# Kernel tuning notes

Measured on AMD Instinct MI355X. Metric: run time of the kernel, lower is better.

Reference implementation:

```python
import jax, jax.numpy as jnp
import numpy as np

V, E, H, K, B, T = 32000, 128, 256, 9, 64, 512


def setup_inputs() -> dict:
    key = jax.random.key(0)
    ks = jax.random.split(key, 12)
    text = jax.random.randint(ks[0], (B, T), 1, V, dtype=jnp.int32)
    lens = jax.random.randint(ks[1], (B,), T // 4, T + 1)
    text = jnp.where(jnp.arange(T)[None, :] < lens[:, None], text, 0)  # 0 = PAD
    labels = jax.random.randint(ks[2], (B, T), 0, K, dtype=jnp.int32)
    g = lambda k, shape, s: jax.random.normal(k, shape, jnp.float32) * s
    emb = g(ks[3], (V, E), 0.02)
    Wf, Uf, bf = g(ks[4], (E, 4 * H), 0.05), g(ks[5], (H, 4 * H), 0.05), jnp.zeros((4 * H,), jnp.float32)
    Wb, Ub, bb = g(ks[6], (E, 4 * H), 0.05), g(ks[7], (H, 4 * H), 0.05), jnp.zeros((4 * H,), jnp.float32)
    Wd, bd = g(ks[8], (2 * H, K), 0.05), jnp.zeros((K,), jnp.float32)
    trans = jax.random.uniform(ks[9], (K, K), jnp.float32)
    return dict(text=text, labels=labels, emb=emb, Wf=Wf, Uf=Uf, bf=bf,
                Wb=Wb, Ub=Ub, bb=bb, Wd=Wd, bd=bd, trans=trans)


def _lstm(x, W, U, b):
    # x: [B, T, E]; Keras LSTM gate order i, f, g(cell), o
    Hn = U.shape[0]
    Bn = x.shape[0]

    def step(carry, xt):
        h, c = carry
        z = xt @ W + h @ U + b
        i, f, g, o = jnp.split(z, 4, axis=-1)
        c = jax.nn.sigmoid(f) * c + jax.nn.sigmoid(i) * jnp.tanh(g)
        h = jax.nn.sigmoid(o) * jnp.tanh(c)
        return (h, c), h

    init = (jnp.zeros((Bn, Hn), x.dtype), jnp.zeros((Bn, Hn), x.dtype))
    _, hs = jax.lax.scan(step, init, jnp.swapaxes(x, 0, 1))  # [T, B, H]
    return jnp.swapaxes(hs, 0, 1)


def _crf_log_likelihood(logits, labels, lens, trans):
    # logits: [B, T, K], labels: [B, T] int, lens: [B] int, trans: [K, K]
    Bn, Tn, Kn = logits.shape
    tmask = jnp.arange(Tn)[None, :] < lens[:, None]           # [B, T] valid token
    tmask2 = jnp.arange(1, Tn)[None, :] < lens[:, None]       # [B, T-1] valid transition
    # gold score: unary + binary
    unary = jnp.take_along_axis(logits, labels[..., None], axis=-1)[..., 0]  # [B, T]
    unary_sum = jnp.sum(unary * tmask, axis=-1)
    binary = trans[labels[:, :-1], labels[:, 1:]]             # [B, T-1]
    binary_sum = jnp.sum(binary * tmask2, axis=-1)
    # log partition via forward algorithm (masked scan)
    alpha0 = logits[:, 0]                                     # [B, K]

    def step(alpha, inp):
        logit_t, m_t = inp                                    # [B, K], [B]
        new = jax.nn.logsumexp(alpha[:, :, None] + trans[None], axis=1) + logit_t
        alpha = jnp.where(m_t[:, None], new, alpha)
        return alpha, None

    alpha, _ = jax.lax.scan(step, alpha0,
                            (jnp.swapaxes(logits[:, 1:], 0, 1), tmask2.T))
    log_norm = jax.nn.logsumexp(alpha, axis=-1)               # [B]
    return unary_sum + binary_sum - log_norm


def reference(text, labels, emb, Wf, Uf, bf, Wb, Ub, bb, Wd, bd, trans):
    text_lens = jnp.sum((text != 0).astype(jnp.int32), axis=-1)
    x = emb[text]                                             # [B, T, E]; dropout inactive at inference
    hf = _lstm(x, Wf, Uf, bf)
    hb = _lstm(x[:, ::-1], Wb, Ub, bb)[:, ::-1]
    logits = jnp.concatenate([hf, hb], axis=-1) @ Wd + bd     # [B, T, K]
    ll = _crf_log_likelihood(logits, labels, text_lens, trans)
    return logits, text_lens, ll
```

## Files before the change

### kernel.cpp

```cpp
#include <hip/hip_runtime.h>
#include <math.h>

#define T_LEN  512
#define B_SZ   64
#define E_DIM  128
#define H_DIM  256
#define G4     1024
#define K_TAGS 9
#define HP     268

typedef __bf16 bf16x8 __attribute__((ext_vector_type(8)));
typedef float  f32x4  __attribute__((ext_vector_type(4)));

union BF8 { bf16x8 v; unsigned short u[8]; uint4 q; unsigned long long ull[2]; };

__device__ __forceinline__ unsigned short rne_bf16(float x) {
    unsigned int b = __float_as_uint(x);
    b += 0x7FFFu + ((b >> 16) & 1u);
    return (unsigned short)(b >> 16);
}
__device__ __forceinline__ float bf16_to_f(unsigned short u) {
    return __uint_as_float(((unsigned int)u) << 16);
}
__device__ __forceinline__ float rcpf_(float x)  { return __builtin_amdgcn_rcpf(x); }
__device__ __forceinline__ float sigf(float x)   { return rcpf_(1.0f + __expf(-x)); }
__device__ __forceinline__ float tanhf_(float x) { return fmaf(2.0f, rcpf_(1.0f + __expf(-2.0f * x)), -1.0f); }

__global__ __launch_bounds__(256)
void init_kernel(const int* __restrict__ text, const float* __restrict__ bd,
                 float* __restrict__ out, int* __restrict__ ws_head) {
    const int b   = blockIdx.x;
    const int tid = threadIdx.x;
    float* lb = out + (size_t)b * (T_LEN * K_TAGS);
    for (int i = tid; i < T_LEN * K_TAGS; i += 256) lb[i] = bd[i % K_TAGS];
    int cnt = 0;
    for (int t = tid; t < T_LEN; t += 256) cnt += (text[b * T_LEN + t] != 0) ? 1 : 0;
    __shared__ int red[4];
    for (int off = 32; off > 0; off >>= 1) cnt += __shfl_down(cnt, off);
    if ((tid & 63) == 0) red[tid >> 6] = cnt;
    __syncthreads();
    if (tid == 0) {
        int c = red[0] + red[1] + red[2] + red[3];
        out[(size_t)B_SZ * T_LEN * K_TAGS + b] = (float)c;
        ws_head[b] = c;
    }
}

__global__ __launch_bounds__(64)
void permute_kernel(const float* __restrict__ Wf, const float* __restrict__ Uf, const float* __restrict__ bf_,
                    const float* __restrict__ Wb, const float* __restrict__ Ub, const float* __restrict__ bb,
                    unsigned short* __restrict__ Uc, unsigned short* __restrict__ Wc,
                    float* __restrict__ bperm)
{
    const int colp = blockIdx.x;
    const int dir  = blockIdx.y;
    const float* W = dir ? Wb : Wf;
    const float* U = dir ? Ub : Uf;
    const float* bs = dir ? bb : bf_;
    const int g = colp & 3, u = colp >> 2;
    const int oc = g * 256 + u;
    const int t = threadIdx.x;
    for (int k = t; k < 256; k += 64)
        Uc[((size_t)dir * 1024 + colp) * 256 + k] = rne_bf16(U[(size_t)k * G4 + oc]);
    for (int k = t; k < 128; k += 64)
        Wc[((size_t)dir * 1024 + colp) * 128 + k] = rne_bf16(W[(size_t)k * G4 + oc]);
    if (t == 0) bperm[dir * 1024 + colp] = bs[oc];
}

__global__ __launch_bounds__(512)
void xw_kernel(const int* __restrict__ text, const float* __restrict__ emb,
               const unsigned short* __restrict__ Wc, const float* __restrict__ bperm,
               unsigned short* __restrict__ xwq)
{
    const int t   = blockIdx.x;
    const int dir = blockIdx.y;
    const int tid = threadIdx.x;
    const int w = tid >> 6, l = tid & 63, r = l & 15, q = l >> 4;

    __shared__ unsigned short xs[64][136];
    __shared__ unsigned short wl[256][136];

    {
        const int b = tid >> 3, e0 = (tid & 7) * 16;
        const int tok = text[b * T_LEN + t];
        const float* er = emb + (size_t)tok * E_DIM + e0;
        #pragma unroll
        for (int jj = 0; jj < 16; ++jj) xs[b][e0 + jj] = rne_bf16(er[jj]);
    }

    for (int nc = 0; nc < 4; ++nc) {
        __syncthreads();
        for (int i = tid; i < 256 * 16; i += 512) {
            const int cc = i >> 4, k8 = (i & 15) * 8;
            *(uint4*)&wl[cc][k8] =
                *(const uint4*)&Wc[((size_t)dir * 1024 + 256 * nc + cc) * 128 + k8];
        }
        __syncthreads();

        #pragma unroll
        for (int mt = 0; mt < 2; ++mt) {
            const int ccol = 32 * w + 16 * mt + r;
            const float4 bb4 = *(const float4*)&bperm[dir * 1024 + 256 * nc + 32 * w + 16 * mt + 4 * q];
            f32x4 acc[4];
            #pragma unroll
            for (int nt = 0; nt < 4; ++nt) acc[nt] = (f32x4){bb4.x, bb4.y, bb4.z, bb4.w};
            #pragma unroll
            for (int ks = 0; ks < 4; ++ks) {
                BF8 af; af.q = *(const uint4*)&wl[ccol][32 * ks + 8 * q];
                #pragma unroll
                for (int nt = 0; nt < 4; ++nt) {
                    BF8 bfv; bfv.q = *(const uint4*)&xs[16 * nt + r][32 * ks + 8 * q];
                    acc[nt] = __builtin_amdgcn_mfma_f32_16x16x32_bf16(af.v, bfv.v, acc[nt], 0, 0, 0);
                }
            }
            #pragma unroll
            for (int nt = 0; nt < 4; ++nt) {
                const int quad = 64 * nc + 8 * w + 4 * mt + q;
                unsigned long long pv =
                      (unsigned long long)rne_bf16(acc[nt][0])
                    | ((unsigned long long)rne_bf16(acc[nt][1]) << 16)
                    | ((unsigned long long)rne_bf16(acc[nt][2]) << 32)
                    | ((unsigned long long)rne_bf16(acc[nt][3]) << 48);
                const size_t off = ((((size_t)dir * 4 + nt) * T_LEN + t) * 256 + quad) * 16 + r;
                *(unsigned long long*)&xwq[off * 4] = pv;
            }
        }
    }
}

__global__ __launch_bounds__(512, 1)
void rec_kernel(const unsigned short* __restrict__ Uc,
                unsigned short* __restrict__ xwq)
{
    const int bx  = blockIdx.x;
    const int dir = bx >> 2, bq = bx & 3;
    const int tid = threadIdx.x;
    const int w = tid >> 6, l = tid & 63, r = l & 15, q = l >> 4;

    __shared__ uint4 ulds4[2][4][1024];
    __shared__ unsigned short hlds[2][16][HP];

    const unsigned short* ucb = Uc + (size_t)dir * 1024 * 256;

    BF8 uf[8][5];
    #pragma unroll
    for (int nt = 0; nt < 8; ++nt) {
        const int colp = 128 * w + 16 * nt + r;
        #pragma unroll
        for (int ks = 0; ks < 5; ++ks)
            uf[nt][ks].q = *(const uint4*)&ucb[(size_t)colp * 256 + 32 * ks + 8 * q];
    }
    for (int i = tid; i < 8192; i += 512) {
        const int s = i >> 12, qq = (i >> 10) & 3, colp = i & 1023;
        ulds4[s][qq][colp] =
            *(const uint4*)&ucb[(size_t)colp * 256 + 160 + 32 * s + 8 * qq];
    }
    {
        unsigned int* hz = (unsigned int*)&hlds[0][0][0];
        for (int i = tid; i < 16 * HP / 2; i += 512) hz[i] = 0u;
    }
    float creg[8] = {0.f, 0.f, 0.f, 0.f, 0.f, 0.f, 0.f, 0.f};
    uint4 hpack = make_uint4(0, 0, 0, 0);
    unsigned short* xwb = xwq + (size_t)(dir * 4 + bq) * T_LEN * 16384;
    const size_t hoff = (size_t)(((w * 4 + q) * 16 + r) * 8);
    __syncthreads();

    for (int t = 0; t < T_LEN; ++t) {
        const int Rb = t & 1, Wn = Rb ^ 1;

        if (t > 0)
            *(uint4*)&xwb[(size_t)(t - 1) * 16384 + hoff] = hpack;

        #pragma unroll
        for (int gr = 0; gr < 2; ++gr) {
            uint2 xwv[4];
            BF8   u7[4];
            #pragma unroll
            for (int nn = 0; nn < 4; ++nn) {
                const int nt = 4 * gr + nn;
                const int quad = 32 * w + 4 * nt + q;
                xwv[nn] = *(const uint2*)&xwb[(size_t)t * 16384 + (size_t)(quad * 16 + r) * 4];
                const int colp = 128 * w + 16 * nt + r;
                u7[nn].q = *(const uint4*)&ucb[(size_t)colp * 256 + 224 + 8 * q];
            }

            f32x4 acc[4];
            #pragma unroll
            for (int nn = 0; nn < 4; ++nn) acc[nn] = (f32x4){0.f, 0.f, 0.f, 0.f};
            #pragma unroll
            for (int ks = 0; ks < 5; ++ks) {
                BF8 hfv; hfv.q = *(const uint4*)&hlds[Rb][r][32 * ks + 8 * q];
                #pragma unroll
                for (int nn = 0; nn < 4; ++nn)
                    acc[nn] = __builtin_amdgcn_mfma_f32_16x16x32_bf16(
                        uf[4 * gr + nn][ks].v, hfv.v, acc[nn], 0, 0, 0);
            }
            #pragma unroll
            for (int ks = 5; ks < 7; ++ks) {
                BF8 hfv; hfv.q = *(const uint4*)&hlds[Rb][r][32 * ks + 8 * q];
                #pragma unroll
                for (int nn = 0; nn < 4; ++nn) {
                    const int colp = 128 * w + 16 * (4 * gr + nn) + r;
                    BF8 uv; uv.q = ulds4[ks - 5][q][colp];
                    acc[nn] = __builtin_amdgcn_mfma_f32_16x16x32_bf16(uv.v, hfv.v, acc[nn], 0, 0, 0);
                }
            }
            {
                BF8 hfv; hfv.q = *(const uint4*)&hlds[Rb][r][224 + 8 * q];
                #pragma unroll
                for (int nn = 0; nn < 4; ++nn)
                    acc[nn] = __builtin_amdgcn_mfma_f32_16x16x32_bf16(
                        u7[nn].v, hfv.v, acc[nn], 0, 0, 0);
            }

            unsigned int p0 = 0, p1 = 0;
            #pragma unroll
            for (int nn = 0; nn < 4; ++nn) {
                const int nt = 4 * gr + nn;
                const uint2 xv = xwv[nn];
                const float z0 = acc[nn][0] + bf16_to_f((unsigned short)(xv.x & 0xffff));
                const float z1 = acc[nn][1] + bf16_to_f((unsigned short)(xv.x >> 16));
                const float z2 = acc[nn][2] + bf16_to_f((unsigned short)(xv.y & 0xffff));
                const float z3 = acc[nn][3] + bf16_to_f((unsigned short)(xv.y >> 16));
                const float c = sigf(z1) * creg[nt] + sigf(z0) * tanhf_(z2);
                const float h = sigf(z3) * tanhf_(c);
                creg[nt] = c;
                const unsigned short hh = rne_bf16(h);
                hlds[Wn][r][32 * w + 4 * nt + q] = hh;
                if (nn < 2) p0 |= ((unsigned int)hh) << (16 * (nn & 1));
                else        p1 |= ((unsigned int)hh) << (16 * (nn & 1));
            }
            if (gr == 0) { hpack.x = p0; hpack.y = p1; }
            else         { hpack.z = p0; hpack.w = p1; }
        }
        __syncthreads();
    }
    *(uint4*)&xwb[(size_t)(T_LEN - 1) * 16384 + hoff] = hpack;
}

__global__ __launch_bounds__(256)
void logits_kernel(const unsigned short* __restrict__ xwq,
                   const float* __restrict__ Wd, const float* __restrict__ bd,
                   float* __restrict__ out)
{
    __shared__ float wdl[2 * H_DIM * K_TAGS];
    __shared__ float bdl[16];
    const int tid = threadIdx.x;
    for (int i = tid; i < 2 * H_DIM * K_TAGS; i += 256) wdl[i] = Wd[i];
    if (tid < K_TAGS) bdl[tid] = bd[tid];
    __syncthreads();

    const int flat = blockIdx.x * 256 + tid;
    const int b = flat >> 9, t = flat & (T_LEN - 1);
    const int bq = b >> 4, bl = b & 15;
    const unsigned short* hf = xwq + ((size_t)(0 * 4 + bq) * T_LEN + t) * 16384;
    const unsigned short* hb = xwq + ((size_t)(1 * 4 + bq) * T_LEN + (T_LEN - 1 - t)) * 16384;

    float a[K_TAGS];
    #pragma unroll
    for (int k = 0; k < K_TAGS; ++k) a[k] = bdl[k];
    #pragma unroll
    for (int w = 0; w < 8; ++w) {
        #pragma unroll
        for (int q = 0; q < 4; ++q) {
            BF8 hv; hv.q = *(const uint4*)&hf[((w * 4 + q) * 16 + bl) * 8];
            #pragma unroll
            for (int nt = 0; nt < 8; ++nt) {
                const float h = bf16_to_f(hv.u[nt]);
                const float* wr = &wdl[(32 * w + 4 * nt + q) * K_TAGS];
                #pragma unroll
                for (int k = 0; k < K_TAGS; ++k) a[k] = fmaf(h, wr[k], a[k]);
            }
        }
    }
    #pragma unroll
    for (int w = 0; w < 8; ++w) {
        #pragma unroll
        for (int q = 0; q < 4; ++q) {
            BF8 hv; hv.q = *(const uint4*)&hb[((w * 4 + q) * 16 + bl) * 8];
            #pragma unroll
            for (int nt = 0; nt < 8; ++nt) {
                const float h = bf16_to_f(hv.u[nt]);
                const float* wr = &wdl[(H_DIM + 32 * w + 4 * nt + q) * K_TAGS];
                #pragma unroll
                for (int k = 0; k < K_TAGS; ++k) a[k] = fmaf(h, wr[k], a[k]);
            }
        }
    }
    float* ob = out + ((size_t)b * T_LEN + t) * K_TAGS;
    #pragma unroll
    for (int k = 0; k < K_TAGS; ++k) ob[k] = a[k];
}

__global__ __launch_bounds__(1024)
void lstm_fb(const int* __restrict__ text, const float* __restrict__ emb,
             const float* __restrict__ Wf, const float* __restrict__ Uf, const float* __restrict__ bf_,
             const float* __restrict__ Wb, const float* __restrict__ Ub, const float* __restrict__ bb,
             const float* __restrict__ Wd, float* __restrict__ out)
{
    const int bi   = blockIdx.x;
    const int d    = bi >> 5;
    const int pair = bi & 31;
    const int tid  = threadIdx.x;
    const int kc   = tid >> 8;
    const int idx  = tid & 255;

    const float* Wp = d ? Wb : Wf;
    const float* Up = d ? Ub : Uf;
    const float* bp = d ? bb : bf_;

    __shared__ __align__(16) float2 vbuf[2][384];
    __shared__ float  cspf[2][H_DIM];
    __shared__ __align__(16) float2 zp[16][256];
    __shared__ float  wdl[H_DIM * K_TAGS];
    __shared__ float  bpl[G4];

    for (int i = tid; i < H_DIM * K_TAGS; i += 1024) wdl[i] = Wd[d * H_DIM * K_TAGS + i];
    for (int i = tid; i < G4; i += 1024) bpl[i] = bp[i];
    if (tid < H_DIM) {
        vbuf[0][E_DIM + tid] = make_float2(0.0f, 0.0f);
        cspf[0][tid] = 0.0f;
        cspf[1][tid] = 0.0f;
    }
    __syncthreads();

    int cur = 0;
    for (int t = 0; t < T_LEN; ++t) {
        const int p = d ? (T_LEN - 1 - t) : t;
        const int nxt = cur ^ 1;

        if (tid < E_DIM) {
            const int tok0 = text[(pair * 2 + 0) * T_LEN + p];
            const int tok1 = text[(pair * 2 + 1) * T_LEN + p];
            vbuf[cur][tid] = make_float2(emb[(size_t)tok0 * E_DIM + tid],
                                         emb[(size_t)tok1 * E_DIM + tid]);
        }
        __syncthreads();

        {
            float2 a0 = make_float2(0.f, 0.f), a1 = a0, a2 = a0, a3 = a0;
            const int k0 = kc * 96;
            const float* wp = Wp + (size_t)k0 * G4 + 4 * idx;
            const float* up = Up + ((long)k0 - E_DIM) * G4 + 4 * idx;
            const float2* __restrict__ vb = vbuf[cur];
            #pragma unroll 8
            for (int i = 0; i < 96; ++i) {
                const int k = k0 + i;
                const float4 wv = *(const float4*)((k < E_DIM) ? wp : up);
                const float2 v = vb[k];
                a0.x = fmaf(wv.x, v.x, a0.x); a0.y = fmaf(wv.x, v.y, a0.y);
                a1.x = fmaf(wv.y, v.x, a1.x); a1.y = fmaf(wv.y, v.y, a1.y);
                a2.x = fmaf(wv.z, v.x, a2.x); a2.y = fmaf(wv.z, v.y, a2.y);
                a3.x = fmaf(wv.w, v.x, a3.x); a3.y = fmaf(wv.w, v.y, a3.y);
                wp += G4; up += G4;
            }
            zp[kc * 4 + 0][idx] = a0;
            zp[kc * 4 + 1][idx] = a1;
            zp[kc * 4 + 2][idx] = a2;
            zp[kc * 4 + 3][idx] = a3;
        }
        __syncthreads();

        if (tid < 512) {
            const int b = tid >> 8, u = tid & 255;
            const int j = u & 3, rr = u >> 2;
            float zs[4];
            #pragma unroll
            for (int g = 0; g < 4; ++g) {
                float s = bpl[g * 256 + u];
                #pragma unroll
                for (int c = 0; c < 4; ++c)
                    s += ((const float*)&zp[c * 4 + j][g * 64 + rr])[b];
                zs[g] = s;
            }
            const float co = cspf[b][u];
            const float cg = tanhf_(zs[2]);
            const float cn = sigf(zs[1]) * co + sigf(zs[0]) * cg;
            const float h  = sigf(zs[3]) * tanhf_(cn);
            cspf[b][u] = cn;
            ((float*)&vbuf[nxt][E_DIM + u])[b] = h;
        }
        __syncthreads();

        {
            const int w = tid >> 6, l = tid & 63;
            const float2* __restrict__ hb = vbuf[nxt] + E_DIM;
            for (int tau = w; tau < 2 * K_TAGS; tau += 16) {
                const int gb = tau / K_TAGS, k = tau - K_TAGS * gb;
                float v = 0.0f;
                #pragma unroll
                for (int m = 0; m < 4; ++m) {
                    const int col = l + 64 * m;
                    const float hv = ((const float*)&hb[col])[gb];
                    v += hv * wdl[col * K_TAGS + k];
                }
                for (int off = 32; off > 0; off >>= 1) v += __shfl_down(v, off);
                if (l == 0)
                    atomicAdd(&out[((size_t)(pair * 2 + gb) * T_LEN + p) * K_TAGS + k], v);
            }
        }
        cur = nxt;
    }
}

__global__ __launch_bounds__(64)
void crf_kernel(const int* __restrict__ labels, const float* __restrict__ trans,
                const int* __restrict__ lens_ws, float* __restrict__ out)
{
    const int b    = blockIdx.x;
    const int lane = threadIdx.x;
    const int len  = lens_ws[b];
    const float* lb = out + (size_t)b * (T_LEN * K_TAGS);
    const int* lab  = labels + (size_t)b * T_LEN;

    float ub = 0.0f;
    for (int t = lane; t < T_LEN; t += 64) {
        if (t < len)            ub += lb[t * K_TAGS + lab[t]];
        if (t >= 1 && t < len)  ub += trans[lab[t - 1] * K_TAGS + lab[t]];
    }
    for (int off = 32; off > 0; off >>= 1) ub += __shfl_down(ub, off);

    float trc[K_TAGS];
    #pragma unroll
    for (int i = 0; i < K_TAGS; ++i)
        trc[i] = (lane < K_TAGS) ? trans[i * K_TAGS + lane] : 0.0f;
    const int kk = (lane < K_TAGS) ? lane : 0;
    float alpha = (lane < K_TAGS) ? lb[lane] : 0.0f;

    for (int t = 1; t < len; ++t) {
        float v[K_TAGS];
        float m = -1e30f;
        #pragma unroll
        for (int i = 0; i < K_TAGS; ++i) {
            float ai = __shfl(alpha, i);
            v[i] = ai + trc[i];
            m = fmaxf(m, v[i]);
        }
        float s = 0.0f;
        #pragma unroll
        for (int i = 0; i < K_TAGS; ++i) s += __expf(v[i] - m);
        float na = m + __logf(s) + lb[t * K_TAGS + kk];
        if (lane < K_TAGS) alpha = na;
    }

    float m2 = -1e30f;
    #pragma unroll
    for (int i = 0; i < K_TAGS; ++i) m2 = fmaxf(m2, __shfl(alpha, i));
    float s2 = 0.0f;
    #pragma unroll
    for (int i = 0; i < K_TAGS; ++i) s2 += __expf(__shfl(alpha, i) - m2);
    float logn = m2 + __logf(s2);

    if (lane == 0)
        out[(size_t)B_SZ * T_LEN * K_TAGS + B_SZ + b] = ub - logn;
}

extern "C" void kernel_launch(void* const* d_in, const int* in_sizes, int n_in,
                              void* d_out, int out_size, void* d_ws, size_t ws_size,
                              hipStream_t stream) {
    const int*   text   = (const int*)d_in[0];
    const int*   labels = (const int*)d_in[1];
    const float* emb    = (const float*)d_in[2];
    const float* Wf     = (const float*)d_in[3];
    const float* Uf     = (const float*)d_in[4];
    const float* bf_    = (const float*)d_in[5];
    const float* Wb     = (const float*)d_in[6];
    const float* Ub     = (const float*)d_in[7];
    const float* bb     = (const float*)d_in[8];
    const float* Wd     = (const float*)d_in[9];
    const float* bd     = (const float*)d_in[10];
    const float* trans  = (const float*)d_in[11];
    float* out = (float*)d_out;

    int* ws_head = (int*)d_ws;
    int* lens_ws = ws_head;

    unsigned short* Uc    = (unsigned short*)((char*)d_ws + 4096);
    unsigned short* Wc    = (unsigned short*)((char*)d_ws + 4096 + 1048576);
    float*          bperm = (float*)((char*)d_ws + 4096 + 1048576 + 524288);
    unsigned short* xwq   = (unsigned short*)((char*)d_ws + 2097152);
    const size_t need = 2097152 + (size_t)2 * 4 * T_LEN * 16384 * 2;

    init_kernel<<<B_SZ, 256, 0, stream>>>(text, bd, out, ws_head);
    if (ws_size >= need) {
        permute_kernel<<<dim3(1024, 2), 64, 0, stream>>>(Wf, Uf, bf_, Wb, Ub, bb, Uc, Wc, bperm);
        xw_kernel<<<dim3(T_LEN, 2), 512, 0, stream>>>(text, emb, Wc, bperm, xwq);
        rec_kernel<<<8, 512, 0, stream>>>(Uc, xwq);
        logits_kernel<<<(B_SZ * T_LEN) / 256, 256, 0, stream>>>(xwq, Wd, bd, out);
    } else {
        lstm_fb<<<64, 1024, 0, stream>>>(text, emb, Wf, Uf, bf_, Wb, Ub, bb, Wd, out);
    }
    crf_kernel<<<B_SZ, 64, 0, stream>>>(labels, trans, lens_ws, out);
}
```

Baseline: 1.567 ms.

## Prefetch next-step xW, fold log2e into weights, seed MFMA accumulators, lighter barrier

Pre-scales the gate weights and biases by log2(e), or 2·log2(e) for the cell gate, during permutation. This lets the recurrence use raw exp2 instead of expf with scaling. The precomputed input projection for step t+1 is loaded into registers during step t, using double-buffered register arrays over an unrolled-by-two loop, and is used as the initial MFMA accumulator instead of being added afterwards. The per-step __syncthreads is replaced by an explicit LDS waitcnt plus s_barrier, which no longer waits on global stores. This risks higher register pressure and slightly different rounding from scaling before bf16 conversion.

```diff
diff --git a/kernel.cpp b/kernel.cpp
--- a/kernel.cpp
+++ b/kernel.cpp
@@ -9,6 +9,9 @@
 #define K_TAGS 9
 #define HP     268
 
+#define L2E      1.442695041f
+#define TWO_L2E  2.885390082f
+
 typedef __bf16 bf16x8 __attribute__((ext_vector_type(8)));
 typedef float  f32x4  __attribute__((ext_vector_type(4)));
 
@@ -23,6 +26,17 @@
     return __uint_as_float(((unsigned int)u) << 16);
 }
 __device__ __forceinline__ float rcpf_(float x)  { return __builtin_amdgcn_rcpf(x); }
+
+__device__ __forceinline__ float exp2n_(float x) {
+#if __has_builtin(__builtin_amdgcn_exp2f)
+    return __builtin_amdgcn_exp2f(-x);
+#else
+    float r; asm("v_exp_f32 %0, -%1" : "=v"(r) : "v"(x)); return r;
+#endif
+}
+__device__ __forceinline__ float sig2_(float zp)  { return rcpf_(1.0f + exp2n_(zp)); }
+__device__ __forceinline__ float tanh2_(float zp) { return fmaf(2.0f, rcpf_(1.0f + exp2n_(zp)), -1.0f); }
+
 __device__ __forceinline__ float sigf(float x)   { return rcpf_(1.0f + __expf(-x)); }
 __device__ __forceinline__ float tanhf_(float x) { return fmaf(2.0f, rcpf_(1.0f + __expf(-2.0f * x)), -1.0f); }
 
@@ -59,12 +73,13 @@
     const float* bs = dir ? bb : bf_;
     const int g = colp & 3, u = colp >> 2;
     const int oc = g * 256 + u;
+    const float sc = (g == 2) ? TWO_L2E : L2E;
     const int t = threadIdx.x;
     for (int k = t; k < 256; k += 64)
-        Uc[((size_t)dir * 1024 + colp) * 256 + k] = rne_bf16(U[(size_t)k * G4 + oc]);
+        Uc[((size_t)dir * 1024 + colp) * 256 + k] = rne_bf16(sc * U[(size_t)k * G4 + oc]);
     for (int k = t; k < 128; k += 64)
-        Wc[((size_t)dir * 1024 + colp) * 128 + k] = rne_bf16(W[(size_t)k * G4 + oc]);
-    if (t == 0) bperm[dir * 1024 + colp] = bs[oc];
+        Wc[((size_t)dir * 1024 + colp) * 128 + k] = rne_bf16(sc * W[(size_t)k * G4 + oc]);
+    if (t == 0) bperm[dir * 1024 + colp] = sc * bs[oc];
 }
 
 __global__ __launch_bounds__(512)
@@ -163,78 +178,101 @@
     uint4 hpack = make_uint4(0, 0, 0, 0);
     unsigned short* xwb = xwq + (size_t)(dir * 4 + bq) * T_LEN * 16384;
     const size_t hoff = (size_t)(((w * 4 + q) * 16 + r) * 8);
+
+    uint2 xwvA[8], xwvB[8];
+    #pragma unroll
+    for (int nt = 0; nt < 8; ++nt) {
+        const int quad = 32 * w + 4 * nt + q;
+        xwvA[nt] = *(const uint2*)&xwb[(size_t)(quad * 16 + r) * 4];
+    }
     __syncthreads();
 
-    for (int t = 0; t < T_LEN; ++t) {
-        const int Rb = t & 1, Wn = Rb ^ 1;
-
-        if (t > 0)
-            *(uint4*)&xwb[(size_t)(t - 1) * 16384 + hoff] = hpack;
-
-        #pragma unroll
-        for (int gr = 0; gr < 2; ++gr) {
-            uint2 xwv[4];
-            BF8   u7[4];
-            #pragma unroll
-            for (int nn = 0; nn < 4; ++nn) {
-                const int nt = 4 * gr + nn;
-                const int quad = 32 * w + 4 * nt + q;
-                xwv[nn] = *(const uint2*)&xwb[(size_t)t * 16384 + (size_t)(quad * 16 + r) * 4];
-                const int colp = 128 * w + 16 * nt + r;
-                u7[nn].q = *(const uint4*)&ucb[(size_t)colp * 256 + 224 + 8 * q];
-            }
-
-            f32x4 acc[4];
-            #pragma unroll
-            for (int nn = 0; nn < 4; ++nn) acc[nn] = (f32x4){0.f, 0.f, 0.f, 0.f};
-            #pragma unroll
-            for (int ks = 0; ks < 5; ++ks) {
-                BF8 hfv; hfv.q = *(const uint4*)&hlds[Rb][r][32 * ks + 8 * q];
-                #pragma unroll
-                for (int nn = 0; nn < 4; ++nn)
-                    acc[nn] = __builtin_amdgcn_mfma_f32_16x16x32_bf16(
-                        uf[4 * gr + nn][ks].v, hfv.v, acc[nn], 0, 0, 0);
-            }
-            #pragma unroll
-            for (int ks = 5; ks < 7; ++ks) {
-                BF8 hfv; hfv.q = *(const uint4*)&hlds[Rb][r][32 * ks + 8 * q];
-                #pragma unroll
-                for (int nn = 0; nn < 4; ++nn) {
-                    const int colp = 128 * w + 16 * (4 * gr + nn) + r;
-                    BF8 uv; uv.q = ulds4[ks - 5][q][colp];
-                    acc[nn] = __builtin_amdgcn_mfma_f32_16x16x32_bf16(uv.v, hfv.v, acc[nn], 0, 0, 0);
-                }
-            }
-            {
-                BF8 hfv; hfv.q = *(const uint4*)&hlds[Rb][r][224 + 8 * q];
-                #pragma unroll
-                for (int nn = 0; nn < 4; ++nn)
-                    acc[nn] = __builtin_amdgcn_mfma_f32_16x16x32_bf16(
-                        u7[nn].v, hfv.v, acc[nn], 0, 0, 0);
-            }
-
-            unsigned int p0 = 0, p1 = 0;
-            #pragma unroll
-            for (int nn = 0; nn < 4; ++nn) {
-                const int nt = 4 * gr + nn;
-                const uint2 xv = xwv[nn];
-                const float z0 = acc[nn][0] + bf16_to_f((unsigned short)(xv.x & 0xffff));
-                const float z1 = acc[nn][1] + bf16_to_f((unsigned short)(xv.x >> 16));
-                const float z2 = acc[nn][2] + bf16_to_f((unsigned short)(xv.y & 0xffff));
-                const float z3 = acc[nn][3] + bf16_to_f((unsigned short)(xv.y >> 16));
-                const float c = sigf(z1) * creg[nt] + sigf(z0) * tanhf_(z2);
-                const float h = sigf(z3) * tanhf_(c);
-                creg[nt] = c;
-                const unsigned short hh = rne_bf16(h);
-                hlds[Wn][r][32 * w + 4 * nt + q] = hh;
-                if (nn < 2) p0 |= ((unsigned int)hh) << (16 * (nn & 1));
-                else        p1 |= ((unsigned int)hh) << (16 * (nn & 1));
-            }
-            if (gr == 0) { hpack.x = p0; hpack.y = p1; }
-            else         { hpack.z = p0; hpack.w = p1; }
-        }
-        __syncthreads();
-    }
+#define REC_STEP(T, XC, XN)                                                         \
+  {                                                                                 \
+    const int Rb_ = (T) & 1, Wn_ = Rb_ ^ 1;                                         \
+    if ((T) > 0)                                                                    \
+        *(uint4*)&xwb[(size_t)((T) - 1) * 16384 + hoff] = hpack;                    \
+    if ((T) + 1 < T_LEN) {                                                          \
+        _Pragma("unroll")                                                           \
+        for (int nt = 0; nt < 8; ++nt) {                                            \
+            const int quad = 32 * w + 4 * nt + q;                                   \
+            XN[nt] = *(const uint2*)&xwb[(size_t)((T) + 1) * 16384                  \
+                                         + (size_t)(quad * 16 + r) * 4];            \
+        }                                                                           \
+    }                                                                               \
+    _Pragma("unroll")                                                               \
+    for (int gr = 0; gr < 2; ++gr) {                                                \
+        BF8 u7[4];                                                                  \
+        _Pragma("unroll")                                                           \
+        for (int nn = 0; nn < 4; ++nn) {                                            \
+            const int colp = 128 * w + 16 * (4 * gr + nn) + r;                      \
+            u7[nn].q = *(const uint4*)&ucb[(size_t)colp * 256 + 224 + 8 * q];       \
+        }                                                                           \
+        f32x4 acc[4];                                                               \
+        _Pragma("unroll")                                                           \
+        for (int nn = 0; nn < 4; ++nn) {                                            \
+            const uint2 xv = XC[4 * gr + nn];                                       \
+            acc[nn] = (f32x4){ bf16_to_f((unsigned short)(xv.x & 0xffffu)),         \
+                               bf16_to_f((unsigned short)(xv.x >> 16)),             \
+                               bf16_to_f((unsigned short)(xv.y & 0xffffu)),         \
+                               bf16_to_f((unsigned short)(xv.y >> 16)) };           \
+        }                                                                           \
+        _Pragma("unroll")                                                           \
+        for (int ks = 0; ks < 5; ++ks) {                                            \
+            BF8 hfv; hfv.q = *(const uint4*)&hlds[Rb_][r][32 * ks + 8 * q];         \
+            _Pragma("unroll")                                                       \
+            for (int nn = 0; nn < 4; ++nn)                                          \
+                acc[nn] = __builtin_amdgcn_mfma_f32_16x16x32_bf16(                  \
+                    uf[4 * gr + nn][ks].v, hfv.v, acc[nn], 0, 0, 0);                \
+        }                                                                           \
+        _Pragma("unroll")                                                           \
+        for (int ks = 5; ks < 7; ++ks) {                                            \
+            BF8 hfv; hfv.q = *(const uint4*)&hlds[Rb_][r][32 * ks + 8 * q];         \
+            _Pragma("unroll")                                                       \
+            for (int nn = 0; nn < 4; ++nn) {                                        \
+                const int colp = 128 * w + 16 * (4 * gr + nn) + r;                  \
+                BF8 uv; uv.q = ulds4[ks - 5][q][colp];                              \
+                acc[nn] = __builtin_amdgcn_mfma_f32_16x16x32_bf16(                  \
+                    uv.v, hfv.v, acc[nn], 0, 0, 0);                                 \
+            }                                                                       \
+        }                                                                           \
+        {                                                                           \
+            BF8 hfv; hfv.q = *(const uint4*)&hlds[Rb_][r][224 + 8 * q];             \
+            _Pragma("unroll")                                                       \
+            for (int nn = 0; nn < 4; ++nn)                                          \
+                acc[nn] = __builtin_amdgcn_mfma_f32_16x16x32_bf16(                  \
+                    u7[nn].v, hfv.v, acc[nn], 0, 0, 0);                             \
+        }                                                                           \
+        unsigned int p0 = 0, p1 = 0;                                                \
+        _Pragma("unroll")                                                           \
+        for (int nn = 0; nn < 4; ++nn) {                                            \
+            const int nt = 4 * gr + nn;                                             \
+            const float si = sig2_(acc[nn][0]);                                     \
+            const float sf = sig2_(acc[nn][1]);                                     \
+            const float tg = tanh2_(acc[nn][2]);                                    \
+            const float so = sig2_(acc[nn][3]);                                     \
+            const float c  = sf * creg[nt] + si * tg;                               \
+            const float h  = so * tanh2_(c * TWO_L2E);                              \
+            creg[nt] = c;                                                           \
+            const unsigned short hh = rne_bf16(h);                                  \
+            hlds[Wn_][r][32 * w + 4 * nt + q] = hh;                                 \
+            if (nn < 2) p0 |= ((unsigned int)hh) << (16 * (nn & 1));                \
+            else        p1 |= ((unsigned int)hh) << (16 * (nn & 1));                \
+        }                                                                           \
+        if (gr == 0) { hpack.x = p0; hpack.y = p1; }                                \
+        else         { hpack.z = p0; hpack.w = p1; }                                \
+    }                                                                               \
+    asm volatile("s_waitcnt lgkmcnt(0)" ::: "memory");                              \
+    __builtin_amdgcn_s_barrier();                                                   \
+    asm volatile("" ::: "memory");                                                  \
+  }
+
+    for (int t = 0; t < T_LEN; t += 2) {
+        REC_STEP(t,     xwvA, xwvB);
+        REC_STEP(t + 1, xwvB, xwvA);
+    }
+#undef REC_STEP
+
     *(uint4*)&xwb[(size_t)(T_LEN - 1) * 16384 + hoff] = hpack;
 }
 
```

Result: slower. 2.339 ms (+49.3%).
